# Kernel optimization log

Measured on AMD Instinct MI355X. Metric: run time of the kernel, lower is better.

Reference implementation:

```python
import jax, jax.numpy as jnp
import numpy as np

BN_EPS = 1e-5
NN_CHUNK = 1024  # unknown points processed per distance-matrix tile


def _batch_ids(cnt, total):
    # contiguous per-batch layout -> batch id of each point via cumsum/searchsorted
    return jnp.searchsorted(jnp.cumsum(cnt), jnp.arange(total), side='right')


def three_nn(unknown, known, ub_id, kb_id):
    """Ragged brute-force 3-NN. Returns (squared dists [N,3], global idx [N,3])."""
    N = unknown.shape[0]
    nchunk = N // NN_CHUNK
    u = unknown.reshape(nchunk, NN_CHUNK, 3)
    ub = ub_id.reshape(nchunk, NN_CHUNK)

    def body(args):
        uc, bc = args
        d2 = jnp.sum((uc[:, None, :] - known[None, :, :]) ** 2, axis=-1)  # [chunk, M]
        d2 = jnp.where(bc[:, None] == kb_id[None, :], d2, jnp.inf)  # mask cross-batch pairs
        neg_d, idx = jax.lax.top_k(-d2, 3)
        return -neg_d, idx

    d2, idx = jax.lax.map(body, (u, ub))
    return d2.reshape(N, 3), idx.reshape(N, 3)


def three_interpolate(known_feats, idx, weight):
    # gather [N,3,C] then inverse-distance weighted sum -> [N,C]
    gathered = known_feats[idx]  # [N,3,C]
    return jnp.einsum('nkc,nk->nc', gathered, weight)


def conv_bn_relu(x, W, gamma, beta):
    # 1x1 Conv2d over [1,C,N,1] == pointwise matmul; BN (training stats) over points
    h = x @ W.T  # [N, C_out]
    mean = jnp.mean(h, axis=0)
    var = jnp.mean((h - mean) ** 2, axis=0)  # biased, as torch BN normalization
    h = (h - mean) * jax.lax.rsqrt(var + BN_EPS) * gamma + beta
    return jax.nn.relu(h)


def setup_inputs() -> dict:
    key = jax.random.key(0)
    ks = jax.random.split(key, 10)
    B, Nper, Mper, C1, C2 = 4, 16384, 4096, 128, 256
    N, M = B * Nper, B * Mper
    unknown = jax.random.normal(ks[0], (N, 3), jnp.float32) * 10.0
    known = jax.random.normal(ks[1], (M, 3), jnp.float32) * 10.0
    unknown_feats = jax.random.normal(ks[2], (N, C1), jnp.float32)
    known_feats = jax.random.normal(ks[3], (M, C2), jnp.float32)
    unknown_batch_cnt = jnp.full((B,), Nper, jnp.int32)
    known_batch_cnt = jnp.full((B,), Mper, jnp.int32)
    Cin = C1 + C2  # 384
    W1 = jax.random.normal(ks[4], (256, Cin), jnp.float32) * (1.0 / np.sqrt(Cin))
    W2 = jax.random.normal(ks[5], (256, 256), jnp.float32) * (1.0 / np.sqrt(256))
    g1 = jnp.ones((256,), jnp.float32); b1 = jnp.zeros((256,), jnp.float32)
    g2 = jnp.ones((256,), jnp.float32); b2 = jnp.zeros((256,), jnp.float32)
    return {"unknown": unknown, "unknown_batch_cnt": unknown_batch_cnt,
            "known": known, "known_batch_cnt": known_batch_cnt,
            "unknown_feats": unknown_feats, "known_feats": known_feats,
            "W1": W1, "g1": g1, "b1": b1, "W2": W2, "g2": g2, "b2": b2}


def reference(unknown, unknown_batch_cnt, known, known_batch_cnt,
              unknown_feats, known_feats, W1, g1, b1, W2, g2, b2):
    ub_id = _batch_ids(unknown_batch_cnt, unknown.shape[0])
    kb_id = _batch_ids(known_batch_cnt, known.shape[0])
    dist, idx = three_nn(unknown, known, ub_id, kb_id)  # squared dists, as CUDA kernel
    dist_recip = 1.0 / (dist + 1e-8)
    weight = dist_recip / jnp.sum(dist_recip, axis=-1, keepdims=True)
    interpolated = three_interpolate(known_feats, idx, weight)  # [N, C2]
    new_features = jnp.concatenate([interpolated, unknown_feats], axis=1)  # [N, C2+C1]
    new_features = conv_bn_relu(new_features, W1, g1, b1)
    new_features = conv_bn_relu(new_features, W2, g2, b2)
    return new_features  # [N, 256]
```

## Files before the change

kernel.cpp:

```cpp
#include <hip/hip_runtime.h>
#include <math.h>

typedef __attribute__((ext_vector_type(8))) short short8;
typedef __attribute__((ext_vector_type(4))) float f32x4;

#define INF 3.0e38f
#define BN_EPS 1e-5f

#define NB 1024
#define XMIN (-64.0f)
#define INVW 8.0f
#define PA 192

__device__ __forceinline__ unsigned short f2bf(float x) {
    union { float f; unsigned u; } v; v.f = x;
    unsigned r = v.u + 0x7FFF + ((v.u >> 16) & 1);
    return (unsigned short)(r >> 16);
}
__device__ __forceinline__ float bf2f(unsigned short u) {
    return __uint_as_float(((unsigned)u) << 16);
}
__device__ __forceinline__ unsigned long long shflx_u64(unsigned long long v, int m) {
    int lo = __shfl_xor((int)(unsigned)(v & 0xFFFFFFFFULL), m, 64);
    int hi = __shfl_xor((int)(unsigned)(v >> 32), m, 64);
    return ((unsigned long long)(unsigned)hi << 32) | (unsigned)lo;
}

__global__ __launch_bounds__(256) void hist2_kernel(
    const float* __restrict__ kn, const int* __restrict__ kcnt, int M,
    const float* __restrict__ un, const int* __restrict__ ucnt, int N,
    int B, int* __restrict__ kc, int* __restrict__ qc)
{
    int j = blockIdx.x * 256 + threadIdx.x;
    const float* P; const int* C; int* out; int idx;
    if (j < M) { P = kn; C = kcnt; out = kc; idx = j; }
    else { idx = j - M; if (idx >= N) return; P = un; C = ucnt; out = qc; }
    int cum = 0, bb = 0;
    for (int i = 0; i < B; i++) { int c = C[i]; if (idx >= cum) bb = i; cum += c; }
    float x = P[idx * 3];
    int bi = (int)((x - XMIN) * INVW);
    bi = min(max(bi, 0), NB - 1);
    atomicAdd(&out[bb * NB + bi], 1);
}

__global__ __launch_bounds__(1024) void scan2_kernel(
    const int* __restrict__ kc, int* __restrict__ kbs, int* __restrict__ kcur,
    const int* __restrict__ qc, int* __restrict__ qbs, int* __restrict__ qcur,
    int T)
{
    __shared__ int ts[1024];
    const int* cnt = blockIdx.x ? qc : kc;
    int* bs  = blockIdx.x ? qbs : kbs;
    int* cur = blockIdx.x ? qcur : kcur;

    int tid = threadIdx.x;
    int base = tid * 4;
    int v0 = 0, v1 = 0, v2 = 0, v3 = 0;
    if (base + 0 < T) v0 = cnt[base + 0];
    if (base + 1 < T) v1 = cnt[base + 1];
    if (base + 2 < T) v2 = cnt[base + 2];
    if (base + 3 < T) v3 = cnt[base + 3];
    int s = v0 + v1 + v2 + v3;
    ts[tid] = s;
    __syncthreads();
    for (int off = 1; off < 1024; off <<= 1) {
        int t = (tid >= off) ? ts[tid - off] : 0;
        __syncthreads();
        ts[tid] += t;
        __syncthreads();
    }
    int ex = ts[tid] - s;
    if (base + 0 < T) { bs[base + 0] = ex; cur[base + 0] = ex; } ex += v0;
    if (base + 1 < T) { bs[base + 1] = ex; cur[base + 1] = ex; } ex += v1;
    if (base + 2 < T) { bs[base + 2] = ex; cur[base + 2] = ex; } ex += v2;
    if (base + 3 < T) { bs[base + 3] = ex; cur[base + 3] = ex; } ex += v3;
    if (tid == ((T - 1) >> 2)) bs[T] = ts[tid];
}

__global__ __launch_bounds__(256) void scatter2_kernel(
    const float* __restrict__ kn, const int* __restrict__ kcnt, int M,
    const float* __restrict__ un, const int* __restrict__ ucnt, int N,
    int B, int* __restrict__ kcur, float4* __restrict__ kscat,
    int* __restrict__ qcur, float4* __restrict__ qscat)
{
    int j = blockIdx.x * 256 + threadIdx.x;
    const float* P; const int* C; int* cur; float4* out; int idx;
    if (j < M) { P = kn; C = kcnt; cur = kcur; out = kscat; idx = j; }
    else { idx = j - M; if (idx >= N) return; P = un; C = ucnt; cur = qcur; out = qscat; }
    int cum = 0, bb = 0;
    for (int i = 0; i < B; i++) { int c = C[i]; if (idx >= cum) bb = i; cum += c; }
    float x = P[idx * 3], y = P[idx * 3 + 1], z = P[idx * 3 + 2];
    int bi = (int)((x - XMIN) * INVW);
    bi = min(max(bi, 0), NB - 1);
    int pos = atomicAdd(&cur[bb * NB + bi], 1);
    out[pos] = make_float4(x, y, z, __int_as_float(idx));
}

__global__ __launch_bounds__(256) void knn11_kernel(
    const int* __restrict__ ucnt, const int* __restrict__ kbs,
    const float4* __restrict__ qscat, const float4* __restrict__ scat,
    int B, int N, float* __restrict__ wgt, int* __restrict__ idxo)
{
    int tid = threadIdx.x;
    int wv = tid >> 6;
    int lane = tid & 63;
    int qi = lane >> 3;
    int r8 = lane & 7;
    int w = blockIdx.x * 4 + wv;
    int qpos = (qi >> 1) * (N >> 2) + w * 2 + (qi & 1);

    int cum = 0, bb = 0;
    for (int i = 0; i < B; i++) { int c = ucnt[i]; if (qpos >= cum) bb = i; cum += c; }

    float4 qf = qscat[qpos];
    float ux = qf.x, uy = qf.y, uz = qf.z;

    int kst = kbs[bb * NB];
    int ken = kbs[bb * NB + NB];

    int bq = (int)((ux - XMIN) * INVW);
    bq = min(max(bq, 0), NB - 1);
    int sp = kbs[bb * NB + bq];

    int abase = sp - PA / 2;
    if (abase + PA > ken) abase = ken - PA;
    if (abase < kst) abase = kst;
    int aend = min(abase + PA, ken);

    float d0 = INF, d1 = INF, d2v = INF;
    auto upd = [&](float e) {
        float m0 = fmaxf(e, d0), m1 = fmaxf(e, d1);
        d0 = fminf(e, d0); d1 = fminf(m0, d1); d2v = fminf(m1, d2v);
    };
    {
        int i = abase + r8;
        for (; i + 24 < aend; i += 32) {
            float e[4];
#pragma unroll
            for (int c = 0; c < 4; c++) {
                float4 f = scat[i + 8 * c];
                float dx = f.x - ux, dy = f.y - uy, dz = f.z - uz;
                e[c] = __builtin_fmaf(dx, dx, __builtin_fmaf(dy, dy, dz * dz));
            }
#pragma unroll
            for (int c = 0; c < 4; c++) upd(e[c]);
        }
        for (; i < aend; i += 8) {
            float4 f = scat[i];
            float dx = f.x - ux, dy = f.y - uy, dz = f.z - uz;
            upd(__builtin_fmaf(dx, dx, __builtin_fmaf(dy, dy, dz * dz)));
        }
    }
#pragma unroll
    for (int s = 1; s <= 4; s <<= 1) {
        float e0 = __shfl_xor(d0, s, 64);
        float e1 = __shfl_xor(d1, s, 64);
        float e2 = __shfl_xor(d2v, s, 64);
        upd(e0); upd(e1); upd(e2);
    }
    float thr = d2v;

    float Wr = fminf(sqrtf(thr), 300.0f);
    int blo = max((int)((ux - Wr - XMIN) * INVW) - 1, 0);
    int bhi = min((int)((ux + Wr - XMIN) * INVW) + 1, NB - 1);
    int pLo = kbs[bb * NB + blo];
    int pHi = kbs[bb * NB + bhi + 1];

    unsigned long long k0 = ~0ULL, k1 = ~0ULL, k2 = ~0ULL;
    auto insK = [&](unsigned long long k) {
        bool cc0 = k < k0;
        unsigned long long t0 = cc0 ? k : k0;
        unsigned long long t1 = cc0 ? k0 : k;
        bool cc1 = t1 < k1;
        unsigned long long u0 = cc1 ? t1 : k1;
        unsigned long long u1 = cc1 ? k1 : t1;
        k0 = t0; k1 = u0;
        k2 = u1 < k2 ? u1 : k2;
    };

    int i = pLo + r8;
    for (; i + 56 < pHi; i += 64) {
        float e[8]; int ix[8];
#pragma unroll
        for (int c = 0; c < 8; c++) {
            float4 f = scat[i + 8 * c];
            float dx = f.x - ux, dy = f.y - uy, dz = f.z - uz;
            e[c] = __builtin_fmaf(dx, dx, __builtin_fmaf(dy, dy, dz * dz));
            ix[c] = __float_as_int(f.w);
        }
        float m4a = fminf(fminf(e[0], e[1]), fminf(e[2], e[3]));
        float m4b = fminf(fminf(e[4], e[5]), fminf(e[6], e[7]));
        if (m4a <= thr) {
#pragma unroll
            for (int c = 0; c < 4; c++) {
                if (e[c] <= thr) {
                    insK(((unsigned long long)__float_as_uint(e[c]) << 32) |
                         (unsigned)ix[c]);
                    thr = fminf(thr, __uint_as_float((unsigned)(k2 >> 32)));
                }
            }
        }
        if (m4b <= thr) {
#pragma unroll
            for (int c = 4; c < 8; c++) {
                if (e[c] <= thr) {
                    insK(((unsigned long long)__float_as_uint(e[c]) << 32) |
                         (unsigned)ix[c]);
                    thr = fminf(thr, __uint_as_float((unsigned)(k2 >> 32)));
                }
            }
        }
    }
    for (; i < pHi; i += 8) {
        float4 f = scat[i];
        float dx = f.x - ux, dy = f.y - uy, dz = f.z - uz;
        float e = __builtin_fmaf(dx, dx, __builtin_fmaf(dy, dy, dz * dz));
        if (e <= thr) {
            insK(((unsigned long long)__float_as_uint(e) << 32) |
                 (unsigned)__float_as_int(f.w));
            thr = fminf(thr, __uint_as_float((unsigned)(k2 >> 32)));
        }
    }

#pragma unroll
    for (int s = 1; s <= 4; s <<= 1) {
        unsigned long long e0 = shflx_u64(k0, s);
        unsigned long long e1 = shflx_u64(k1, s);
        unsigned long long e2 = shflx_u64(k2, s);
        insK(e0); insK(e1); insK(e2);
    }

    if (r8 == 0) {
        float dd0 = __uint_as_float((unsigned)(k0 >> 32));
        float dd1 = __uint_as_float((unsigned)(k1 >> 32));
        float dd2 = __uint_as_float((unsigned)(k2 >> 32));
        float r0 = 1.0f / (dd0 + 1e-8f);
        float r1 = 1.0f / (dd1 + 1e-8f);
        float r2 = 1.0f / (dd2 + 1e-8f);
        float rs = 1.0f / (r0 + r1 + r2);
        int orig = __float_as_int(qf.w);
        wgt[orig * 3 + 0] = r0 * rs;
        wgt[orig * 3 + 1] = r1 * rs;
        wgt[orig * 3 + 2] = r2 * rs;
        idxo[orig * 3 + 0] = (int)(unsigned)k0;
        idxo[orig * 3 + 1] = (int)(unsigned)k1;
        idxo[orig * 3 + 2] = (int)(unsigned)k2;
    }
}

__global__ __launch_bounds__(256) void interp_kernel(
    const float* __restrict__ kfeat, const float* __restrict__ wgt,
    const int* __restrict__ idxv, unsigned short* __restrict__ Ab)
{
    int tid = threadIdx.x;
    int row = blockIdx.x * 8 + (tid >> 5);
    int ch = (tid & 31) * 8;
    float w0 = wgt[row * 3 + 0], w1 = wgt[row * 3 + 1], w2 = wgt[row * 3 + 2];
    int j0 = idxv[row * 3 + 0], j1 = idxv[row * 3 + 1], j2 = idxv[row * 3 + 2];
    const float* f0 = kfeat + (size_t)j0 * 256 + ch;
    const float* f1 = kfeat + (size_t)j1 * 256 + ch;
    const float* f2 = kfeat + (size_t)j2 * 256 + ch;
    float4 x0 = *(const float4*)f0, x1 = *(const float4*)(f0 + 4);
    float4 y0 = *(const float4*)f1, y1 = *(const float4*)(f1 + 4);
    float4 z0 = *(const float4*)f2, z1 = *(const float4*)(f2 + 4);
    ushort4 o0, o1;
    o0.x = f2bf(x0.x * w0 + y0.x * w1 + z0.x * w2);
    o0.y = f2bf(x0.y * w0 + y0.y * w1 + z0.y * w2);
    o0.z = f2bf(x0.z * w0 + y0.z * w1 + z0.z * w2);
    o0.w = f2bf(x0.w * w0 + y0.w * w1 + z0.w * w2);
    o1.x = f2bf(x1.x * w0 + y1.x * w1 + z1.x * w2);
    o1.y = f2bf(x1.y * w0 + y1.y * w1 + z1.y * w2);
    o1.z = f2bf(x1.z * w0 + y1.z * w1 + z1.z * w2);
    o1.w = f2bf(x1.w * w0 + y1.w * w1 + z1.w * w2);
    unsigned short* dst = Ab + (size_t)row * 256 + ch;
    *(ushort4*)dst = o0;
    *(ushort4*)(dst + 4) = o1;
}

__global__ __launch_bounds__(256) void wconv_kernel(
    const float* __restrict__ W1, const float* __restrict__ W2,
    unsigned short* __restrict__ W1b, unsigned short* __restrict__ W2b,
    int n1, int n2)
{
    int i = blockIdx.x * 256 + threadIdx.x;
    if (i < n1) W1b[i] = f2bf(W1[i]);
    int j = i - n1;
    if (j >= 0 && j < n2) W2b[j] = f2bf(W2[j]);
}

template <int K, int MODE>
__global__ __launch_bounds__(256) void gemm_bf16_kernel(
    const void* __restrict__ Aa, const float* __restrict__ ufeat,
    const unsigned short* __restrict__ W,
    const float* __restrict__ bnsum, const float* __restrict__ bnsq,
    const float* __restrict__ bng, const float* __restrict__ bnb, float invN,
    void* __restrict__ Cv, float* __restrict__ gsum, float* __restrict__ gsq)
{
    __shared__ unsigned short As[128 * 40];
    __shared__ unsigned short Bs[128 * 40];
    __shared__ float colsum[128];
    __shared__ float colsq[128];
    __shared__ float sc[256], sh[256];

    int tid = threadIdx.x;
    int w = tid >> 6, lane = tid & 63;
    int r = w >> 1, cq = w & 1;
    int m16 = lane & 15, q = lane >> 4;
    int bm = blockIdx.x * 128, bn = blockIdx.y * 128;

    if (MODE == 1) {
        float mean = bnsum[tid] * invN;
        float var = bnsq[tid] * invN - mean * mean;
        float scv = bng[tid] * rsqrtf(var + BN_EPS);
        sc[tid] = scv;
        sh[tid] = bnb[tid] - mean * scv;
    }

    int srow = tid >> 2;
    int kc = (tid & 3) * 8;

    f32x4 acc[4][4];
#pragma unroll
    for (int i = 0; i < 4; i++)
#pragma unroll
        for (int j = 0; j < 4; j++) acc[i][j] = (f32x4){0.f, 0.f, 0.f, 0.f};

#pragma unroll
    for (int k0 = 0; k0 < K; k0 += 32) {
        __syncthreads();
#pragma unroll
        for (int t = 0; t < 2; t++) {
            int row = srow + 64 * t;
            int c = k0 + kc;
            if (MODE == 0) {
                if (c < 256) {
                    *(short8*)&As[row * 40 + kc] = *(const short8*)(
                        (const unsigned short*)Aa + (size_t)(bm + row) * 256 + c);
                } else {
                    const float* fu = ufeat + (size_t)(bm + row) * 128 + (c - 256);
                    float4 u0 = *(const float4*)fu, u1 = *(const float4*)(fu + 4);
                    ushort4 o0, o1;
                    o0.x = f2bf(u0.x); o0.y = f2bf(u0.y);
                    o0.z = f2bf(u0.z); o0.w = f2bf(u0.w);
                    o1.x = f2bf(u1.x); o1.y = f2bf(u1.y);
                    o1.z = f2bf(u1.z); o1.w = f2bf(u1.w);
                    *(ushort4*)&As[row * 40 + kc] = o0;
                    *(ushort4*)&As[row * 40 + kc + 4] = o1;
                }
            } else {
                const unsigned short* Ab = (const unsigned short*)Aa;
                ushort4 h0 = *(const ushort4*)(Ab + (size_t)(bm + row) * K + c);
                ushort4 h1v = *(const ushort4*)(Ab + (size_t)(bm + row) * K + c + 4);
                float4 s0 = *(const float4*)&sc[c];
                float4 s1 = *(const float4*)&sc[c + 4];
                float4 t0 = *(const float4*)&sh[c];
                float4 t1 = *(const float4*)&sh[c + 4];
                ushort4 o0, o1;
                o0.x = f2bf(fmaxf(bf2f(h0.x) * s0.x + t0.x, 0.f));
                o0.y = f2bf(fmaxf(bf2f(h0.y) * s0.y + t0.y, 0.f));
                o0.z = f2bf(fmaxf(bf2f(h0.z) * s0.z + t0.z, 0.f));
                o0.w = f2bf(fmaxf(bf2f(h0.w) * s0.w + t0.w, 0.f));
                o1.x = f2bf(fmaxf(bf2f(h1v.x) * s1.x + t1.x, 0.f));
                o1.y = f2bf(fmaxf(bf2f(h1v.y) * s1.y + t1.y, 0.f));
                o1.z = f2bf(fmaxf(bf2f(h1v.z) * s1.z + t1.z, 0.f));
                o1.w = f2bf(fmaxf(bf2f(h1v.w) * s1.w + t1.w, 0.f));
                *(ushort4*)&As[row * 40 + kc] = o0;
                *(ushort4*)&As[row * 40 + kc + 4] = o1;
            }
            *(short8*)&Bs[row * 40 + kc] =
                *(const short8*)(W + (size_t)(bn + row) * K + k0 + kc);
        }
        __syncthreads();

        short8 af[4], bf[4];
#pragma unroll
        for (int sub = 0; sub < 4; sub++) {
            af[sub] = *(const short8*)&As[(r * 64 + sub * 16 + m16) * 40 + q * 8];
            bf[sub] = *(const short8*)&Bs[(cq * 64 + sub * 16 + m16) * 40 + q * 8];
        }
#pragma unroll
        for (int sm = 0; sm < 4; sm++)
#pragma unroll
            for (int sn = 0; sn < 4; sn++)
                acc[sm][sn] = __builtin_amdgcn_mfma_f32_16x16x32_bf16(
                    af[sm], bf[sn], acc[sm][sn], 0, 0, 0);
    }

    int row0 = bm + r * 64 + q * 4;
    int col0 = bn + cq * 64 + m16;
#pragma unroll
    for (int sm = 0; sm < 4; sm++)
#pragma unroll
        for (int sn = 0; sn < 4; sn++) {
            f32x4 v = acc[sm][sn];
#pragma unroll
            for (int reg = 0; reg < 4; reg++) {
                size_t idx = (size_t)(row0 + sm * 16 + reg) * 256 + col0 + sn * 16;
                if (MODE == 0) ((unsigned short*)Cv)[idx] = f2bf(v[reg]);
                else           ((float*)Cv)[idx] = v[reg];
            }
        }

    __syncthreads();
    if (tid < 128) { colsum[tid] = 0.f; colsq[tid] = 0.f; }
    __syncthreads();
#pragma unroll
    for (int sn = 0; sn < 4; sn++) {
        float sacc = 0.f, qacc = 0.f;
#pragma unroll
        for (int sm = 0; sm < 4; sm++) {
            f32x4 v = acc[sm][sn];
#pragma unroll
            for (int reg = 0; reg < 4; reg++) {
                sacc += v[reg];
                qacc += v[reg] * v[reg];
            }
        }
        int lc = cq * 64 + sn * 16 + m16;
        atomicAdd(&colsum[lc], sacc);
        atomicAdd(&colsq[lc], qacc);
    }
    __syncthreads();
    if (tid < 128) {
        atomicAdd(&gsum[bn + tid], colsum[tid]);
        atomicAdd(&gsq[bn + tid], colsq[tid]);
    }
}

__global__ __launch_bounds__(256) void final_act_kernel(
    const float* __restrict__ h2, const float* __restrict__ bnsum,
    const float* __restrict__ bnsq, const float* __restrict__ bng,
    const float* __restrict__ bnb, float invN,
    float* __restrict__ out, int total4)
{
    __shared__ float sc[256], sh[256];
    int c = threadIdx.x;
    float mean = bnsum[c] * invN;
    float var = bnsq[c] * invN - mean * mean;
    float scv = bng[c] * rsqrtf(var + BN_EPS);
    sc[c] = scv;
    sh[c] = bnb[c] - mean * scv;
    __syncthreads();

    int i = blockIdx.x * 256 + threadIdx.x;
    if (i >= total4) return;
    int c4 = i & 63;
    float4 v = ((const float4*)h2)[i];
    float4 s = *(const float4*)&sc[c4 * 4];
    float4 t = *(const float4*)&sh[c4 * 4];
    float4 o;
    o.x = fmaxf(v.x * s.x + t.x, 0.0f);
    o.y = fmaxf(v.y * s.y + t.y, 0.0f);
    o.z = fmaxf(v.z * s.z + t.z, 0.0f);
    o.w = fmaxf(v.w * s.w + t.w, 0.0f);
    ((float4*)out)[i] = o;
}

extern "C" void kernel_launch(void* const* d_in, const int* in_sizes, int n_in,
                              void* d_out, int out_size, void* d_ws, size_t ws_size,
                              hipStream_t stream)
{
    const float* unknown = (const float*)d_in[0];
    const int*   ucnt    = (const int*)d_in[1];
    const float* known   = (const float*)d_in[2];
    const int*   kcnt    = (const int*)d_in[3];
    const float* ufeat   = (const float*)d_in[4];
    const float* kfeat   = (const float*)d_in[5];
    const float* W1      = (const float*)d_in[6];
    const float* g1      = (const float*)d_in[7];
    const float* b1      = (const float*)d_in[8];
    const float* W2      = (const float*)d_in[9];
    const float* g2      = (const float*)d_in[10];
    const float* b2      = (const float*)d_in[11];

    int N = in_sizes[0] / 3;
    int B = in_sizes[1];
    int M = in_sizes[2] / 3;
    int T = B * NB;

    char* ws = (char*)d_ws;
    size_t off = 0;
    float* wgt = (float*)(ws + off);            off += (size_t)N * 3 * 4;
    int*   idxb = (int*)(ws + off);             off += (size_t)N * 3 * 4;
    float* stats = (float*)(ws + off);          off += 4 * 256 * 4;
    float* sum1 = stats,        *sq1 = stats + 256;
    float* sum2 = stats + 512,  *sq2 = stats + 768;
    int* kch = (int*)(ws + off);                off += (size_t)T * 4;
    int* qch = (int*)(ws + off);                off += (size_t)T * 4;
    int* kbs = (int*)(ws + off);                off += ((size_t)T + 1) * 4;
    int* qbs = (int*)(ws + off);                off += ((size_t)T + 1) * 4;
    int* kcur = (int*)(ws + off);               off += (size_t)T * 4;
    int* qcur = (int*)(ws + off);               off += (size_t)T * 4;
    unsigned short* W1b = (unsigned short*)(ws + off);  off += 256 * 384 * 2;
    unsigned short* W2b = (unsigned short*)(ws + off);  off += 256 * 256 * 2;
    off = (off + 255) & ~(size_t)255;
    float4* kscat = (float4*)(ws + off);        off += (size_t)M * sizeof(float4);
    float4* qscat = (float4*)(ws + off);        off += (size_t)N * sizeof(float4);
    off = (off + 255) & ~(size_t)255;
    unsigned short* Abuf = (unsigned short*)(ws + off); off += (size_t)N * 256 * 2;
    off = (off + 255) & ~(size_t)255;
    unsigned short* h1 = (unsigned short*)(ws + off);   off += (size_t)N * 256 * 2;
    off = (off + 255) & ~(size_t)255;
    float* h2 = (float*)(ws + off);

    float invN = 1.0f / (float)N;

    hipMemsetAsync(stats, 0, 4 * 256 * 4 + 2 * (size_t)T * 4, stream);

    wconv_kernel<<<(256 * 384 + 256 * 256 + 255) / 256, 256, 0, stream>>>(
        W1, W2, W1b, W2b, 256 * 384, 256 * 256);

    hist2_kernel<<<(M + N + 255) / 256, 256, 0, stream>>>(
        known, kcnt, M, unknown, ucnt, N, B, kch, qch);
    scan2_kernel<<<2, 1024, 0, stream>>>(kch, kbs, kcur, qch, qbs, qcur, T);
    scatter2_kernel<<<(M + N + 255) / 256, 256, 0, stream>>>(
        known, kcnt, M, unknown, ucnt, N, B, kcur, kscat, qcur, qscat);
    knn11_kernel<<<N / 32, 256, 0, stream>>>(ucnt, kbs, qscat, kscat,
                                             B, N, wgt, idxb);

    interp_kernel<<<N / 8, 256, 0, stream>>>(kfeat, wgt, idxb, Abuf);

    gemm_bf16_kernel<384, 0><<<dim3(N / 128, 2), 256, 0, stream>>>(
        Abuf, ufeat, W1b,
        nullptr, nullptr, nullptr, nullptr, 0.f, h1, sum1, sq1);
    gemm_bf16_kernel<256, 1><<<dim3(N / 128, 2), 256, 0, stream>>>(
        h1, nullptr, W2b,
        sum1, sq1, g1, b1, invN, h2, sum2, sq2);
    final_act_kernel<<<N / 4, 256, 0, stream>>>(h2, sum2, sq2, g2, b2, invN,
                                                (float*)d_out, N * 64);
}
```

Measured before the change: 360.9 us.

## Map one query per lane and share wave-uniform candidate windows in kNN

```diff
diff --git a/kernel.cpp b/kernel.cpp
--- a/kernel.cpp
+++ b/kernel.cpp
@@ -19,11 +19,6 @@
 }
 __device__ __forceinline__ float bf2f(unsigned short u) {
     return __uint_as_float(((unsigned)u) << 16);
-}
-__device__ __forceinline__ unsigned long long shflx_u64(unsigned long long v, int m) {
-    int lo = __shfl_xor((int)(unsigned)(v & 0xFFFFFFFFULL), m, 64);
-    int hi = __shfl_xor((int)(unsigned)(v >> 32), m, 64);
-    return ((unsigned long long)(unsigned)hi << 32) | (unsigned)lo;
 }
 
 __global__ __launch_bounds__(256) void hist2_kernel(
@@ -96,75 +91,79 @@
     out[pos] = make_float4(x, y, z, __int_as_float(idx));
 }
 
-__global__ __launch_bounds__(256) void knn11_kernel(
+__global__ __launch_bounds__(256) void knn12_kernel(
     const int* __restrict__ ucnt, const int* __restrict__ kbs,
     const float4* __restrict__ qscat, const float4* __restrict__ scat,
-    int B, int N, float* __restrict__ wgt, int* __restrict__ idxo)
+    int B, float* __restrict__ wgt, int* __restrict__ idxo)
 {
     int tid = threadIdx.x;
-    int wv = tid >> 6;
-    int lane = tid & 63;
-    int qi = lane >> 3;
-    int r8 = lane & 7;
-    int w = blockIdx.x * 4 + wv;
-    int qpos = (qi >> 1) * (N >> 2) + w * 2 + (qi & 1);
+    int wv = tid >> 6, lane = tid & 63;
+    int pbase = blockIdx.x * 256;
+    int qpos = pbase + wv * 64 + lane;
 
     int cum = 0, bb = 0;
-    for (int i = 0; i < B; i++) { int c = ucnt[i]; if (qpos >= cum) bb = i; cum += c; }
+    for (int i = 0; i < B; i++) { int c = ucnt[i]; if (pbase >= cum) bb = i; cum += c; }
 
     float4 qf = qscat[qpos];
     float ux = qf.x, uy = qf.y, uz = qf.z;
 
     int kst = kbs[bb * NB];
     int ken = kbs[bb * NB + NB];
-
-    int bq = (int)((ux - XMIN) * INVW);
-    bq = min(max(bq, 0), NB - 1);
+    int bq = min(max((int)((ux - XMIN) * INVW), 0), NB - 1);
     int sp = kbs[bb * NB + bq];
 
-    int abase = sp - PA / 2;
-    if (abase + PA > ken) abase = ken - PA;
-    if (abase < kst) abase = kst;
-    int aend = min(abase + PA, ken);
+    int spmin = sp, spmax = sp;
+#pragma unroll
+    for (int s = 1; s < 64; s <<= 1) {
+        spmin = min(spmin, __shfl_xor(spmin, s, 64));
+        spmax = max(spmax, __shfl_xor(spmax, s, 64));
+    }
+    int abase = __builtin_amdgcn_readfirstlane(max(spmin - PA / 2, kst));
+    int aend  = __builtin_amdgcn_readfirstlane(min(spmax + PA / 2, ken));
 
     float d0 = INF, d1 = INF, d2v = INF;
     auto upd = [&](float e) {
         float m0 = fmaxf(e, d0), m1 = fmaxf(e, d1);
         d0 = fminf(e, d0); d1 = fminf(m0, d1); d2v = fminf(m1, d2v);
     };
-    {
-        int i = abase + r8;
-        for (; i + 24 < aend; i += 32) {
-            float e[4];
-#pragma unroll
-            for (int c = 0; c < 4; c++) {
-                float4 f = scat[i + 8 * c];
-                float dx = f.x - ux, dy = f.y - uy, dz = f.z - uz;
-                e[c] = __builtin_fmaf(dx, dx, __builtin_fmaf(dy, dy, dz * dz));
-            }
-#pragma unroll
-            for (int c = 0; c < 4; c++) upd(e[c]);
-        }
-        for (; i < aend; i += 8) {
-            float4 f = scat[i];
+
+    for (int i = abase; i < aend; i += 8) {
+#pragma unroll
+        for (int c = 0; c < 8; c++) {
+            int j = i + c;
+            float4 f = scat[min(j, aend - 1)];
             float dx = f.x - ux, dy = f.y - uy, dz = f.z - uz;
-            upd(__builtin_fmaf(dx, dx, __builtin_fmaf(dy, dy, dz * dz)));
-        }
-    }
-#pragma unroll
-    for (int s = 1; s <= 4; s <<= 1) {
-        float e0 = __shfl_xor(d0, s, 64);
-        float e1 = __shfl_xor(d1, s, 64);
-        float e2 = __shfl_xor(d2v, s, 64);
-        upd(e0); upd(e1); upd(e2);
+            float e = __builtin_fmaf(dx, dx, __builtin_fmaf(dy, dy, dz * dz));
+            upd(j < aend ? e : INF);
+        }
     }
     float thr = d2v;
 
     float Wr = fminf(sqrtf(thr), 300.0f);
     int blo = max((int)((ux - Wr - XMIN) * INVW) - 1, 0);
     int bhi = min((int)((ux + Wr - XMIN) * INVW) + 1, NB - 1);
-    int pLo = kbs[bb * NB + blo];
-    int pHi = kbs[bb * NB + bhi + 1];
+    int wlo = kbs[bb * NB + blo];
+    int whi = kbs[bb * NB + bhi + 1];
+#pragma unroll
+    for (int s = 1; s < 64; s <<= 1) {
+        wlo = min(wlo, __shfl_xor(wlo, s, 64));
+        whi = max(whi, __shfl_xor(whi, s, 64));
+    }
+    wlo = __builtin_amdgcn_readfirstlane(wlo);
+    whi = __builtin_amdgcn_readfirstlane(whi);
+
+    d0 = INF; d1 = INF; d2v = INF;
+    for (int i = wlo; i < whi; i += 8) {
+#pragma unroll
+        for (int c = 0; c < 8; c++) {
+            int j = i + c;
+            float4 f = scat[min(j, whi - 1)];
+            float dx = f.x - ux, dy = f.y - uy, dz = f.z - uz;
+            float e = __builtin_fmaf(dx, dx, __builtin_fmaf(dy, dy, dz * dz));
+            upd(j < whi ? e : INF);
+        }
+    }
+    float d3 = d2v;
 
     unsigned long long k0 = ~0ULL, k1 = ~0ULL, k2 = ~0ULL;
     auto insK = [&](unsigned long long k) {
@@ -178,74 +177,44 @@
         k2 = u1 < k2 ? u1 : k2;
     };
 
-    int i = pLo + r8;
-    for (; i + 56 < pHi; i += 64) {
+    for (int i = wlo; i < whi; i += 8) {
         float e[8]; int ix[8];
 #pragma unroll
         for (int c = 0; c < 8; c++) {
-            float4 f = scat[i + 8 * c];
+            int j = i + c;
+            float4 f = scat[min(j, whi - 1)];
             float dx = f.x - ux, dy = f.y - uy, dz = f.z - uz;
-            e[c] = __builtin_fmaf(dx, dx, __builtin_fmaf(dy, dy, dz * dz));
+            float ev = __builtin_fmaf(dx, dx, __builtin_fmaf(dy, dy, dz * dz));
+            e[c] = (j < whi) ? ev : INF;
             ix[c] = __float_as_int(f.w);
         }
-        float m4a = fminf(fminf(e[0], e[1]), fminf(e[2], e[3]));
-        float m4b = fminf(fminf(e[4], e[5]), fminf(e[6], e[7]));
-        if (m4a <= thr) {
-#pragma unroll
-            for (int c = 0; c < 4; c++) {
-                if (e[c] <= thr) {
+        float m8 = fminf(fminf(fminf(e[0], e[1]), fminf(e[2], e[3])),
+                         fminf(fminf(e[4], e[5]), fminf(e[6], e[7])));
+        if (m8 <= d3) {
+#pragma unroll
+            for (int c = 0; c < 8; c++) {
+                if (e[c] <= d3) {
                     insK(((unsigned long long)__float_as_uint(e[c]) << 32) |
                          (unsigned)ix[c]);
-                    thr = fminf(thr, __uint_as_float((unsigned)(k2 >> 32)));
                 }
             }
         }
-        if (m4b <= thr) {
-#pragma unroll
-            for (int c = 4; c < 8; c++) {
-                if (e[c] <= thr) {
-                    insK(((unsigned long long)__float_as_uint(e[c]) << 32) |
-                         (unsigned)ix[c]);
-                    thr = fminf(thr, __uint_as_float((unsigned)(k2 >> 32)));
-                }
-            }
-        }
-    }
-    for (; i < pHi; i += 8) {
-        float4 f = scat[i];
-        float dx = f.x - ux, dy = f.y - uy, dz = f.z - uz;
-        float e = __builtin_fmaf(dx, dx, __builtin_fmaf(dy, dy, dz * dz));
-        if (e <= thr) {
-            insK(((unsigned long long)__float_as_uint(e) << 32) |
-                 (unsigned)__float_as_int(f.w));
-            thr = fminf(thr, __uint_as_float((unsigned)(k2 >> 32)));
-        }
-    }
-
-#pragma unroll
-    for (int s = 1; s <= 4; s <<= 1) {
-        unsigned long long e0 = shflx_u64(k0, s);
-        unsigned long long e1 = shflx_u64(k1, s);
-        unsigned long long e2 = shflx_u64(k2, s);
-        insK(e0); insK(e1); insK(e2);
-    }
-
-    if (r8 == 0) {
-        float dd0 = __uint_as_float((unsigned)(k0 >> 32));
-        float dd1 = __uint_as_float((unsigned)(k1 >> 32));
-        float dd2 = __uint_as_float((unsigned)(k2 >> 32));
-        float r0 = 1.0f / (dd0 + 1e-8f);
-        float r1 = 1.0f / (dd1 + 1e-8f);
-        float r2 = 1.0f / (dd2 + 1e-8f);
-        float rs = 1.0f / (r0 + r1 + r2);
-        int orig = __float_as_int(qf.w);
-        wgt[orig * 3 + 0] = r0 * rs;
-        wgt[orig * 3 + 1] = r1 * rs;
-        wgt[orig * 3 + 2] = r2 * rs;
-        idxo[orig * 3 + 0] = (int)(unsigned)k0;
-        idxo[orig * 3 + 1] = (int)(unsigned)k1;
-        idxo[orig * 3 + 2] = (int)(unsigned)k2;
-    }
+    }
+
+    float dd0 = __uint_as_float((unsigned)(k0 >> 32));
+    float dd1 = __uint_as_float((unsigned)(k1 >> 32));
+    float dd2 = __uint_as_float((unsigned)(k2 >> 32));
+    float r0 = 1.0f / (dd0 + 1e-8f);
+    float r1 = 1.0f / (dd1 + 1e-8f);
+    float r2 = 1.0f / (dd2 + 1e-8f);
+    float rs = 1.0f / (r0 + r1 + r2);
+    int orig = __float_as_int(qf.w);
+    wgt[orig * 3 + 0] = r0 * rs;
+    wgt[orig * 3 + 1] = r1 * rs;
+    wgt[orig * 3 + 2] = r2 * rs;
+    idxo[orig * 3 + 0] = (int)(unsigned)k0;
+    idxo[orig * 3 + 1] = (int)(unsigned)k1;
+    idxo[orig * 3 + 2] = (int)(unsigned)k2;
 }
 
 __global__ __launch_bounds__(256) void interp_kernel(
@@ -515,8 +484,8 @@
     scan2_kernel<<<2, 1024, 0, stream>>>(kch, kbs, kcur, qch, qbs, qcur, T);
     scatter2_kernel<<<(M + N + 255) / 256, 256, 0, stream>>>(
         known, kcnt, M, unknown, ucnt, N, B, kcur, kscat, qcur, qscat);
-    knn11_kernel<<<N / 32, 256, 0, stream>>>(ucnt, kbs, qscat, kscat,
-                                             B, N, wgt, idxb);
+    knn12_kernel<<<N / 256, 256, 0, stream>>>(ucnt, kbs, qscat, kscat,
+                                              B, wgt, idxb);
 
     interp_kernel<<<N / 8, 256, 0, stream>>>(kfeat, wgt, idxb, Abuf);
 
```

New measurement: 761.6 us. 111% more time.
